# Kernel optimization log

Hardware: AMD Instinct MI355X
Metric: run time of the kernel (lower is better)

The kernel has to match this reference:

```python
import jax, jax.numpy as jnp
import numpy as np
import math

B, N, D, H = 16, 200, 2048, 2048  # batch, seq (== max_len), feature dim, hidden/output dim


def setup_inputs() -> dict:
    key = jax.random.key(0)
    ks = jax.random.split(key, 16)
    s = 1.0 / math.sqrt(D)
    return {
        "input_query": jax.random.normal(ks[0], (B, N, D), jnp.float32),
        "input_key": jax.random.normal(ks[1], (B, N, D), jnp.float32),
        "input_value": jax.random.normal(ks[2], (B, N, D), jnp.float32),
        "loc_vector": jax.random.normal(ks[3], (B, N, D), jnp.float32),
        "Wq": jax.random.normal(ks[4], (D, H), jnp.float32) * s,
        "bq": jnp.zeros((H,), jnp.float32),
        "Wk": jax.random.normal(ks[5], (D, H), jnp.float32) * s,
        "bk": jnp.zeros((H,), jnp.float32),
        "Wv": jax.random.normal(ks[6], (D, H), jnp.float32) * s,
        "bv": jnp.zeros((H,), jnp.float32),
        "Wloc": jax.random.normal(ks[7], (D, H), jnp.float32) * s,
        "bloc": jnp.zeros((H,), jnp.float32),
        "Wlk": jax.random.normal(ks[8], (D, H), jnp.float32) * s,
        "blk": jnp.zeros((H,), jnp.float32),
        "param": jax.random.normal(ks[9], (B, N, H), jnp.float32),
    }


def reference(input_query, input_key, input_value, loc_vector,
              Wq, bq, Wk, bk, Wv, bv, Wloc, bloc, Wlk, blk, param):
    n = input_query.shape[1]
    lq = input_query @ Wq + bq                      # (b, n, h)
    lk = input_key @ Wk + bk                        # (b, m, h)
    lv = input_value @ Wv + bv                      # (b, m, o)
    loc = loc_vector[:, :n, :]
    lloc = loc @ Wloc + bloc                        # (b, n, h)
    kloc = loc @ Wlk + blk                          # (b, n, h)
    p = param[: input_query.shape[0], :n, :]        # (b, n, h)
    # Fused multi-term scores: (Q+P)K^T + (Q+Lloc)Kloc^T  == QK^T + Lloc Kloc^T + P K^T + Q Kloc^T
    scores = (jnp.einsum('bnh,bmh->bnm', lq + p, lk)
              + jnp.einsum('bnh,bmh->bnm', lq + lloc, kloc))
    attn = jax.nn.softmax(scores / math.sqrt(lq.shape[-1]), axis=-1)
    return jnp.einsum('bnm,bmo->bno', attn, lv)     # (b, n, o); dropout is identity in eval
```

## Files before the change

kernel.cpp:

```cpp
#include <hip/hip_runtime.h>
#include <hip/hip_bf16.h>
#include <math.h>

typedef float floatx4 __attribute__((ext_vector_type(4)));
typedef __bf16 bf16x8 __attribute__((ext_vector_type(8)));
typedef unsigned short ushort_t;

__device__ __forceinline__ ushort_t f2bf(float f) {
    union { float f; unsigned int i; } v; v.f = f;
    unsigned int i = v.i;
    return (ushort_t)((i + 0x7FFFu + ((i >> 16) & 1u)) >> 16);
}
__device__ __forceinline__ unsigned int pack2(float a, float b) {
    return (unsigned int)f2bf(a) | ((unsigned int)f2bf(b) << 16);
}
__device__ __forceinline__ floatx4 mfma16(bf16x8 a, bf16x8 b, floatx4 c) {
    return __builtin_amdgcn_mfma_f32_16x16x32_bf16(a, b, c, 0, 0, 0);
}
__device__ __forceinline__ void load_lds16(const ushort_t* g, ushort_t* l) {
    __builtin_amdgcn_global_load_lds(
        (const __attribute__((address_space(1))) unsigned int*)g,
        (__attribute__((address_space(3))) unsigned int*)l, 16, 0, 0);
}

__global__ __launch_bounds__(256) void k_convert(const float* __restrict__ q, const float* __restrict__ k,
                          const float* __restrict__ v, const float* __restrict__ loc,
                          ushort_t* qb, ushort_t* kb, ushort_t* vb, ushort_t* locb) {
    int z = blockIdx.y;
    const float* src = z == 0 ? q : z == 1 ? k : z == 2 ? v : loc;
    ushort_t* dst    = z == 0 ? qb : z == 1 ? kb : z == 2 ? vb : locb;
    size_t idx = (size_t)blockIdx.x * 256 + threadIdx.x;
    floatx4 f = *(const floatx4*)(src + idx * 4);
    uint2 o;
    o.x = pack2(f[0], f[1]);
    o.y = pack2(f[2], f[3]);
    *(uint2*)(dst + idx * 4) = o;
}

__global__ void k_wtrans(const float* __restrict__ w0, const float* __restrict__ w1,
                         const float* __restrict__ w2, const float* __restrict__ w3,
                         const float* __restrict__ w4,
                         ushort_t* t0, ushort_t* t1, ushort_t* t2, ushort_t* t3, ushort_t* t4) {
    __shared__ float tile[32][33];
    int z = blockIdx.z;
    const float* W = z == 0 ? w0 : z == 1 ? w1 : z == 2 ? w2 : z == 3 ? w3 : w4;
    ushort_t* T    = z == 0 ? t0 : z == 1 ? t1 : z == 2 ? t2 : z == 3 ? t3 : t4;
    int n0 = blockIdx.x * 32, k0 = blockIdx.y * 32;
    int tx = threadIdx.x & 31, ty = threadIdx.x >> 5;
#pragma unroll
    for (int i = 0; i < 4; i++) {
        int row = ty + i * 8;
        tile[row][tx] = W[(size_t)(k0 + row) * 2048 + n0 + tx];
    }
    __syncthreads();
#pragma unroll
    for (int i = 0; i < 4; i++) {
        int row = ty + i * 8;
        T[(size_t)(n0 + row) * 2048 + k0 + tx] = f2bf(tile[tx][row]);
    }
}

__global__ void k_vtrans(const ushort_t* __restrict__ lv, ushort_t* __restrict__ lvT) {
    __shared__ ushort_t tile[32][33];
    int n0 = blockIdx.x * 32;
    int t0 = blockIdx.y * 32;
    int b = blockIdx.z;
    int tx = threadIdx.x & 31, ty = threadIdx.x >> 5;
#pragma unroll
    for (int i = 0; i < 4; i++) {
        int row = ty + i * 8;
        int tk = t0 + row;
        ushort_t v = 0;
        if (tk < 200) v = lv[(size_t)(b * 200 + tk) * 2048 + n0 + tx];
        tile[row][tx] = v;
    }
    __syncthreads();
#pragma unroll
    for (int i = 0; i < 4; i++) {
        int row = ty + i * 8;
        lvT[((size_t)b * 2048 + n0 + row) * 224 + t0 + tx] = tile[tx][row];
    }
}

#define G_SB  __builtin_amdgcn_sched_barrier(0)
#define G_BAR __builtin_amdgcn_s_barrier()

__global__ __launch_bounds__(512, 2) void k_gemm(
    const ushort_t* A0, const ushort_t* A1, const ushort_t* A2, const ushort_t* A3, const ushort_t* A4,
    const ushort_t* W0, const ushort_t* W1, const ushort_t* W2, const ushort_t* W3, const ushort_t* W4,
    const float* B0, const float* B1, const float* B2, const float* B3, const float* B4,
    ushort_t* lqp, ushort_t* lvp, ushort_t* llocp, ushort_t* kcat) {
    int wg = blockIdx.x;
    int swz = (wg & 7) * 65 + (wg >> 3);
    int z = swz / 104;
    int rem = swz - z * 104;
    int ntile = rem / 13;
    int mtile = rem - ntile * 13;
    int m0 = mtile * 256, n0 = ntile * 256;

    const ushort_t* A  = z == 0 ? A0 : z == 1 ? A1 : z == 2 ? A2 : z == 3 ? A3 : A4;
    const ushort_t* Wt = z == 0 ? W0 : z == 1 ? W1 : z == 2 ? W2 : z == 3 ? W3 : W4;
    const float* bias  = z == 0 ? B0 : z == 1 ? B1 : z == 2 ? B2 : z == 3 ? B3 : B4;

    __shared__ ushort_t As[2][256 * 32];
    __shared__ ushort_t Bs[2][256 * 32];

    int tid = threadIdx.x;
    int lane = tid & 63, w = tid >> 6;
    int quad = lane >> 4, col = lane & 15;
    int wr = w >> 2, wc = w & 3;

    int srow = lane >> 2;
    int cch  = (lane & 3) ^ ((lane >> 3) & 3);
    const ushort_t* AgB0 = A  + (size_t)(m0 + (0 * 8 + w) * 16 + srow) * 2048 + cch * 8;
    const ushort_t* AgB1 = A  + (size_t)(m0 + (1 * 8 + w) * 16 + srow) * 2048 + cch * 8;
    const ushort_t* BgB0 = Wt + (size_t)(n0 + (0 * 8 + w) * 16 + srow) * 2048 + cch * 8;
    const ushort_t* BgB1 = Wt + (size_t)(n0 + (1 * 8 + w) * 16 + srow) * 2048 + cch * 8;
    int dst0 = (0 * 8 + w) * 512;
    int dst1 = (1 * 8 + w) * 512;

#define G_STAGE(K0, B) do {                         \
        load_lds16(AgB0 + (K0), As[B] + dst0);      \
        load_lds16(AgB1 + (K0), As[B] + dst1);      \
        load_lds16(BgB0 + (K0), Bs[B] + dst0);      \
        load_lds16(BgB1 + (K0), Bs[B] + dst1);      \
    } while (0)

    int aoff[8], boff[4];
#pragma unroll
    for (int mi = 0; mi < 8; mi++) {
        int row = wr * 128 + mi * 16 + col;
        aoff[mi] = row * 32 + (quad ^ ((row >> 1) & 3)) * 8;
    }
#pragma unroll
    for (int ni = 0; ni < 4; ni++) {
        int row = wc * 64 + ni * 16 + col;
        boff[ni] = row * 32 + (quad ^ ((row >> 1) & 3)) * 8;
    }

    floatx4 acc[8][4] = {};

#define G_COMPUTE(B) do {                                                \
        bf16x8 af[8], bfr[4];                                            \
        _Pragma("unroll") for (int mi = 0; mi < 8; mi++)                 \
            af[mi] = *(const bf16x8*)&As[B][aoff[mi]];                   \
        _Pragma("unroll") for (int ni = 0; ni < 4; ni++)                 \
            bfr[ni] = *(const bf16x8*)&Bs[B][boff[ni]];                  \
        __builtin_amdgcn_s_setprio(1);                                   \
        _Pragma("unroll") for (int mi = 0; mi < 8; mi++)                 \
            _Pragma("unroll") for (int ni = 0; ni < 4; ni++)             \
                acc[mi][ni] = mfma16(af[mi], bfr[ni], acc[mi][ni]);      \
        __builtin_amdgcn_s_setprio(0);                                   \
    } while (0)

    G_STAGE(0, 0);

#pragma unroll 1
    for (int tt = 0; tt < 31; tt++) {
        int k0 = tt * 64;
        G_STAGE(k0 + 32, 1);
        asm volatile("s_waitcnt vmcnt(4)" ::: "memory");
        G_SB; G_BAR; G_SB;
        G_COMPUTE(0);
        G_SB; G_BAR;
        G_STAGE(k0 + 64, 0);
        asm volatile("s_waitcnt vmcnt(4)" ::: "memory");
        G_SB; G_BAR; G_SB;
        G_COMPUTE(1);
        G_SB; G_BAR;
    }
    G_STAGE(2016, 1);
    asm volatile("s_waitcnt vmcnt(4)" ::: "memory");
    G_SB; G_BAR; G_SB;
    G_COMPUTE(0);
    G_SB; G_BAR;
    asm volatile("s_waitcnt vmcnt(0)" ::: "memory");
    G_SB; G_BAR; G_SB;
    G_COMPUTE(1);

    ushort_t* Cplain = z == 0 ? lqp : z == 2 ? lvp : llocp;
    int kcoff = (z == 4) ? 2048 : 0;
    bool to_kcat = (z == 1 || z == 4);
    float bvv[4];
#pragma unroll
    for (int ni = 0; ni < 4; ni++) bvv[ni] = bias[n0 + wc * 64 + ni * 16 + col];
#pragma unroll
    for (int mi = 0; mi < 8; mi++) {
#pragma unroll
        for (int r = 0; r < 4; r++) {
            int m = m0 + wr * 128 + mi * 16 + quad * 4 + r;
            if (m < 3200) {
                ushort_t* crow;
                if (to_kcat) {
                    int bb = m / 200, rr = m - bb * 200;
                    crow = kcat + (size_t)(bb * 224 + rr) * 4096 + kcoff;
                } else {
                    crow = Cplain + (size_t)m * 2048;
                }
#pragma unroll
                for (int ni = 0; ni < 4; ni++) {
                    int n = n0 + wc * 64 + ni * 16 + col;
                    crow[n] = f2bf(acc[mi][ni][r] + bvv[ni]);
                }
            }
        }
    }
#undef G_STAGE
#undef G_COMPUTE
}

__global__ __launch_bounds__(256) void k_qprep(const ushort_t* __restrict__ lqp,
                                               const ushort_t* __restrict__ llocp,
                                               const float* __restrict__ param,
                                               ushort_t* __restrict__ qcat) {
    int m = blockIdx.x;
    int b = m / 200, r = m - b * 200;
    int c = threadIdx.x * 8;
    bf16x8 ql = *(const bf16x8*)(lqp + (size_t)m * 2048 + c);
    bf16x8 ll = *(const bf16x8*)(llocp + (size_t)m * 2048 + c);
    floatx4 p0 = *(const floatx4*)(param + (size_t)m * 2048 + c);
    floatx4 p1 = *(const floatx4*)(param + (size_t)m * 2048 + c + 4);
    bf16x8 q1, q2;
#pragma unroll
    for (int j = 0; j < 4; j++) {
        q1[j]     = (__bf16)((float)ql[j] + p0[j]);
        q1[j + 4] = (__bf16)((float)ql[j + 4] + p1[j]);
        q2[j]     = (__bf16)((float)ql[j] + (float)ll[j]);
        q2[j + 4] = (__bf16)((float)ql[j + 4] + (float)ll[j + 4]);
    }
    ushort_t* dst = qcat + ((size_t)(b * 224 + r)) * 4096 + c;
    *(bf16x8*)dst = q1;
    *(bf16x8*)(dst + 2048) = q2;
}

__global__ __launch_bounds__(256) void k_scores(const ushort_t* __restrict__ qcat,
                                                const ushort_t* __restrict__ kcat,
                                                float* __restrict__ part) {
    int qt = blockIdx.x;
    int b  = blockIdx.y;
    int kc = blockIdx.z;
    __shared__ ushort_t As[32 * 32];
    __shared__ ushort_t Bs[224 * 32];

    int tid = threadIdx.x;
    int lane = tid & 63, w = tid >> 6;
    int quad = lane >> 4, col = lane & 15;
    int srow = lane >> 2, scol = (lane & 3) * 8;

    const ushort_t* qbase = qcat + ((size_t)b * 224 + qt * 32) * 4096 + kc * 2048;
    const ushort_t* kbase = kcat + (size_t)b * 224 * 4096 + kc * 2048;

    const ushort_t* ssrc[4];
    ushort_t* sdst[4];
#pragma unroll
    for (int o = 0; o < 4; o++) {
        int id = w * 4 + o;
        if (id < 14) {
            ssrc[o] = kbase + (size_t)(id * 16 + srow) * 4096 + scol;
            sdst[o] = Bs + id * 512;
        } else {
            ssrc[o] = qbase + (size_t)((id - 14) * 16 + srow) * 4096 + scol;
            sdst[o] = As + (id - 14) * 512;
        }
    }

    floatx4 acc[2][4] = {};
    for (int k0 = 0; k0 < 2048; k0 += 32) {
        __syncthreads();
#pragma unroll
        for (int o = 0; o < 4; o++) load_lds16(ssrc[o] + k0, sdst[o]);
        __syncthreads();
        bf16x8 af[2];
#pragma unroll
        for (int mi = 0; mi < 2; mi++) af[mi] = *(const bf16x8*)&As[(mi * 16 + col) * 32 + quad * 8];
#pragma unroll
        for (int fi = 0; fi < 4; fi++) {
            int f = w + fi * 4;
            if (f < 14) {
                bf16x8 bf = *(const bf16x8*)&Bs[(f * 16 + col) * 32 + quad * 8];
#pragma unroll
                for (int mi = 0; mi < 2; mi++) acc[mi][fi] = mfma16(af[mi], bf, acc[mi][fi]);
            }
        }
    }

    float* pbase = part + ((size_t)(kc * 16 + b) * 224 + qt * 32) * 224;
#pragma unroll
    for (int fi = 0; fi < 4; fi++) {
        int f = w + fi * 4;
        if (f < 14) {
#pragma unroll
            for (int mi = 0; mi < 2; mi++)
#pragma unroll
                for (int r = 0; r < 4; r++)
                    pbase[(mi * 16 + quad * 4 + r) * 224 + f * 16 + col] = acc[mi][fi][r];
        }
    }
}

__global__ __launch_bounds__(256) void k_softmax(const float* __restrict__ part,
                                                 ushort_t* __restrict__ attn) {
    int row = blockIdx.x * 8 + (threadIdx.x >> 5);
    int b = row / 200, r = row - b * 200;
    int p = threadIdx.x & 31;
    const float* p0 = part + ((size_t)b * 224 + r) * 224;
    const float* p1 = p0 + (size_t)16 * 224 * 224;
    const float scale = 0.022097086912079608f;
    float ev[7];
    float mx = -1e30f;
#pragma unroll
    for (int j = 0; j < 7; j++) {
        int c = p * 7 + j;
        float v = (c < 200) ? (p0[c] + p1[c]) * scale : -1e30f;
        ev[j] = v;
        mx = fmaxf(mx, v);
    }
#pragma unroll
    for (int m = 1; m < 32; m <<= 1) mx = fmaxf(mx, __shfl_xor(mx, m, 32));
    float s = 0.f;
#pragma unroll
    for (int j = 0; j < 7; j++) {
        float e = __expf(ev[j] - mx);
        ev[j] = e;
        s += e;
    }
#pragma unroll
    for (int m = 1; m < 32; m <<= 1) s += __shfl_xor(s, m, 32);
    float rs = 1.0f / s;
    ushort_t* arow = attn + (size_t)row * 224;
#pragma unroll
    for (int j = 0; j < 7; j++) {
        int c = p * 7 + j;
        arow[c] = (c < 200) ? f2bf(ev[j] * rs) : (ushort_t)0;
    }
}

__global__ __launch_bounds__(256) void k_pv(const ushort_t* __restrict__ attn,
                                            const ushort_t* __restrict__ lvT,
                                            float* __restrict__ out) {
    int nt = blockIdx.x;
    int qt = blockIdx.y;
    int b = blockIdx.z;
    int tid = threadIdx.x, lane = tid & 63, w = tid >> 6;
    int quad = lane >> 4, col = lane & 15;
    int aq = qt * 16 + col; if (aq > 199) aq = 199;
    const ushort_t* arow = attn + (size_t)(b * 200 + aq) * 224;
    int nbase = nt * 128 + w * 32;
    const ushort_t* bp0 = lvT + ((size_t)b * 2048 + nbase + col) * 224;
    const ushort_t* bp1 = lvT + ((size_t)b * 2048 + nbase + 16 + col) * 224;
    floatx4 acc[2] = {};
#pragma unroll
    for (int k0 = 0; k0 < 224; k0 += 32) {
        int ko = k0 + quad * 8;
        bf16x8 av = *(const bf16x8*)(arow + ko);
        bf16x8 b0 = *(const bf16x8*)(bp0 + ko);
        bf16x8 b1 = *(const bf16x8*)(bp1 + ko);
        acc[0] = mfma16(av, b0, acc[0]);
        acc[1] = mfma16(av, b1, acc[1]);
    }
#pragma unroll
    for (int f = 0; f < 2; f++) {
        int n = nbase + f * 16 + col;
#pragma unroll
        for (int r = 0; r < 4; r++) {
            int m = qt * 16 + quad * 4 + r;
            if (m < 200) out[(size_t)(b * 200 + m) * 2048 + n] = acc[f][r];
        }
    }
}

extern "C" void kernel_launch(void* const* d_in, const int* in_sizes, int n_in,
                              void* d_out, int out_size, void* d_ws, size_t ws_size,
                              hipStream_t stream) {
    (void)in_sizes; (void)n_in; (void)out_size; (void)ws_size;
    const float* q    = (const float*)d_in[0];
    const float* k    = (const float*)d_in[1];
    const float* v    = (const float*)d_in[2];
    const float* loc  = (const float*)d_in[3];
    const float* Wq   = (const float*)d_in[4];
    const float* bq   = (const float*)d_in[5];
    const float* Wk   = (const float*)d_in[6];
    const float* bk   = (const float*)d_in[7];
    const float* Wv   = (const float*)d_in[8];
    const float* bv   = (const float*)d_in[9];
    const float* Wloc = (const float*)d_in[10];
    const float* bloc = (const float*)d_in[11];
    const float* Wlk  = (const float*)d_in[12];
    const float* blk  = (const float*)d_in[13];
    const float* param = (const float*)d_in[14];
    float* out = (float*)d_out;

    size_t off = 0;
    auto nxt = [&](size_t bytes) {
        void* p = (char*)d_ws + off;
        off += (bytes + 255) & ~(size_t)255;
        return p;
    };
    ushort_t* wt[5];
    for (int i = 0; i < 5; i++) wt[i] = (ushort_t*)nxt(2048ull * 2048 * 2);
    ushort_t* qb    = (ushort_t*)nxt(3200ull * 2048 * 2);
    ushort_t* kb    = (ushort_t*)nxt(3200ull * 2048 * 2);
    ushort_t* vb    = (ushort_t*)nxt(3200ull * 2048 * 2);
    ushort_t* locb  = (ushort_t*)nxt(3200ull * 2048 * 2);
    ushort_t* lqp   = (ushort_t*)nxt(3200ull * 2048 * 2);
    ushort_t* llocp = (ushort_t*)nxt(3200ull * 2048 * 2);
    ushort_t* lvp   = (ushort_t*)nxt(3200ull * 2048 * 2);
    ushort_t* kcat  = (ushort_t*)nxt(16ull * 224 * 4096 * 2);
    ushort_t* lvT  = wt[0];
    ushort_t* attn = wt[0] + 16ull * 2048 * 224;
    float*    part = (float*)((char*)d_ws + 2ull * 2048 * 2048 * 2);
    ushort_t* qcat = qb;

    k_convert<<<dim3(6400, 4), 256, 0, stream>>>(q, k, v, loc, qb, kb, vb, locb);
    k_wtrans<<<dim3(64, 64, 5), 256, 0, stream>>>(Wq, Wk, Wv, Wloc, Wlk,
                                                  wt[0], wt[1], wt[2], wt[3], wt[4]);
    k_gemm<<<dim3(520), 512, 0, stream>>>(qb, kb, vb, locb, locb,
                                          wt[0], wt[1], wt[2], wt[3], wt[4],
                                          bq, bk, bv, bloc, blk,
                                          lqp, lvp, llocp, kcat);
    k_qprep<<<dim3(3200), 256, 0, stream>>>(lqp, llocp, param, qcat);
    k_vtrans<<<dim3(64, 7, 16), 256, 0, stream>>>(lvp, lvT);
    k_scores<<<dim3(7, 16, 2), 256, 0, stream>>>(qcat, kcat, part);
    k_softmax<<<dim3(400), 256, 0, stream>>>(part, attn);
    k_pv<<<dim3(16, 13, 16), 256, 0, stream>>>(attn, lvT, out);
}
```

Measured before the change: 515.8 us.

## Restructure projection GEMM main loop into 64-wide K tiles with quadrant-split pipeline

The projection GEMM now stages 64-wide K tiles instead of 32-wide ones, using an XOR swizzle across 8 chunks. Each K step is split into four quadrant MFMA phases, with LDS fragment reads and partial global-to-LDS loads for the next tiles interleaved between barriers. The aim is to overlap LDS reads and global loads with MFMA work and to halve the number of loop iterations. In exchange there are more barriers per iteration, LDS use doubles (which may limit the 2 blocks/CU occupancy), and the asynchronous buffer reuse carries correctness risk. The wraparound tile indices issue a few redundant loads at the tail.

Result: slower. 535.5 us (+3.8%).

```diff
diff --git a/kernel.cpp b/kernel.cpp
--- a/kernel.cpp
+++ b/kernel.cpp
@@ -82,8 +82,12 @@
     }
 }
 
-#define G_SB  __builtin_amdgcn_sched_barrier(0)
-#define G_BAR __builtin_amdgcn_s_barrier()
+#define G_SB   __builtin_amdgcn_sched_barrier(0)
+#define G_BAR  __builtin_amdgcn_s_barrier()
+#define WAITL0 asm volatile("s_waitcnt lgkmcnt(0)" ::: "memory")
+#define WAITL8 asm volatile("s_waitcnt lgkmcnt(8)" ::: "memory")
+#define WVM4   asm volatile("s_waitcnt vmcnt(4)" ::: "memory")
+#define WVM0   asm volatile("s_waitcnt vmcnt(0)" ::: "memory")
 
 __global__ __launch_bounds__(512, 2) void k_gemm(
     const ushort_t* A0, const ushort_t* A1, const ushort_t* A2, const ushort_t* A3, const ushort_t* A4,
@@ -102,81 +106,99 @@
     const ushort_t* Wt = z == 0 ? W0 : z == 1 ? W1 : z == 2 ? W2 : z == 3 ? W3 : W4;
     const float* bias  = z == 0 ? B0 : z == 1 ? B1 : z == 2 ? B2 : z == 3 ? B3 : B4;
 
-    __shared__ ushort_t As[2][256 * 32];
-    __shared__ ushort_t Bs[2][256 * 32];
+    __shared__ ushort_t AsF[2 * 256 * 64];
+    __shared__ ushort_t BsF[2 * 256 * 64];
 
     int tid = threadIdx.x;
     int lane = tid & 63, w = tid >> 6;
     int quad = lane >> 4, col = lane & 15;
     int wr = w >> 2, wc = w & 3;
 
-    int srow = lane >> 2;
-    int cch  = (lane & 3) ^ ((lane >> 3) & 3);
-    const ushort_t* AgB0 = A  + (size_t)(m0 + (0 * 8 + w) * 16 + srow) * 2048 + cch * 8;
-    const ushort_t* AgB1 = A  + (size_t)(m0 + (1 * 8 + w) * 16 + srow) * 2048 + cch * 8;
-    const ushort_t* BgB0 = Wt + (size_t)(n0 + (0 * 8 + w) * 16 + srow) * 2048 + cch * 8;
-    const ushort_t* BgB1 = Wt + (size_t)(n0 + (1 * 8 + w) * 16 + srow) * 2048 + cch * 8;
-    int dst0 = (0 * 8 + w) * 512;
-    int dst1 = (1 * 8 + w) * 512;
-
-#define G_STAGE(K0, B) do {                         \
-        load_lds16(AgB0 + (K0), As[B] + dst0);      \
-        load_lds16(AgB1 + (K0), As[B] + dst1);      \
-        load_lds16(BgB0 + (K0), Bs[B] + dst0);      \
-        load_lds16(BgB1 + (K0), Bs[B] + dst1);      \
-    } while (0)
-
-    int aoff[8], boff[4];
-#pragma unroll
-    for (int mi = 0; mi < 8; mi++) {
-        int row = wr * 128 + mi * 16 + col;
-        aoff[mi] = row * 32 + (quad ^ ((row >> 1) & 3)) * 8;
-    }
-#pragma unroll
-    for (int ni = 0; ni < 4; ni++) {
-        int row = wc * 64 + ni * 16 + col;
-        boff[ni] = row * 32 + (quad ^ ((row >> 1) & 3)) * 8;
-    }
-
+    int sl = lane >> 3;
+    int sc = ((lane & 7) ^ sl) * 8;
+    const ushort_t* Ag[4]; const ushort_t* Bg[4]; int ldst[4];
+#pragma unroll
+    for (int u = 0; u < 4; u++) {
+        int rowoff = (u >> 1) * 128 + (u & 1) * 64 + w * 8;
+        Ag[u] = A  + (size_t)(m0 + rowoff + sl) * 2048 + sc;
+        Bg[u] = Wt + (size_t)(n0 + rowoff + sl) * 2048 + sc;
+        ldst[u] = rowoff * 64;
+    }
+
+#define STG_A(KT, BUF) do { int kk = (KT) * 64;                       \
+        load_lds16(Ag[0] + kk, AsF + (BUF) * 16384 + ldst[0]);        \
+        load_lds16(Ag[1] + kk, AsF + (BUF) * 16384 + ldst[1]);        \
+        load_lds16(Ag[2] + kk, AsF + (BUF) * 16384 + ldst[2]);        \
+        load_lds16(Ag[3] + kk, AsF + (BUF) * 16384 + ldst[3]); } while (0)
+#define STG_BLO(KT, BUF) do { int kk = (KT) * 64;                     \
+        load_lds16(Bg[0] + kk, BsF + (BUF) * 16384 + ldst[0]);        \
+        load_lds16(Bg[1] + kk, BsF + (BUF) * 16384 + ldst[1]); } while (0)
+#define STG_BHI(KT, BUF) do { int kk = (KT) * 64;                     \
+        load_lds16(Bg[2] + kk, BsF + (BUF) * 16384 + ldst[2]);        \
+        load_lds16(Bg[3] + kk, BsF + (BUF) * 16384 + ldst[3]); } while (0)
+
+    int sw = col & 7;
+    int ko0 = (quad ^ sw) * 8;
+    int ko1 = ((4 | quad) ^ sw) * 8;
+    int aro[8], bro[4];
+#pragma unroll
+    for (int mi = 0; mi < 8; mi++) aro[mi] = (wr * 128 + mi * 16 + col) * 64;
+#pragma unroll
+    for (int ni = 0; ni < 4; ni++) bro[ni] = (wc * 64 + ni * 16 + col) * 64;
+
+    bf16x8 af[4][2], bfr[2][2];
     floatx4 acc[8][4] = {};
 
-#define G_COMPUTE(B) do {                                                \
-        bf16x8 af[8], bfr[4];                                            \
-        _Pragma("unroll") for (int mi = 0; mi < 8; mi++)                 \
-            af[mi] = *(const bf16x8*)&As[B][aoff[mi]];                   \
-        _Pragma("unroll") for (int ni = 0; ni < 4; ni++)                 \
-            bfr[ni] = *(const bf16x8*)&Bs[B][boff[ni]];                  \
-        __builtin_amdgcn_s_setprio(1);                                   \
-        _Pragma("unroll") for (int mi = 0; mi < 8; mi++)                 \
-            _Pragma("unroll") for (int ni = 0; ni < 4; ni++)             \
-                acc[mi][ni] = mfma16(af[mi], bfr[ni], acc[mi][ni]);      \
-        __builtin_amdgcn_s_setprio(0);                                   \
-    } while (0)
-
-    G_STAGE(0, 0);
+#define RD_A(J, MI, BUF) do {                                         \
+        const ushort_t* p_ = AsF + (BUF) * 16384 + aro[MI];           \
+        af[J][0] = *(const bf16x8*)(p_ + ko0);                        \
+        af[J][1] = *(const bf16x8*)(p_ + ko1); } while (0)
+#define RD_B(J, NI, BUF) do {                                         \
+        const ushort_t* p_ = BsF + (BUF) * 16384 + bro[NI];           \
+        bfr[J][0] = *(const bf16x8*)(p_ + ko0);                       \
+        bfr[J][1] = *(const bf16x8*)(p_ + ko1); } while (0)
+#define QMFMA(MH, NB) do {                                            \
+        __builtin_amdgcn_s_setprio(1);                                \
+        _Pragma("unroll") for (int mi = 0; mi < 4; mi++)              \
+        _Pragma("unroll") for (int nj = 0; nj < 2; nj++) {            \
+            acc[(MH) * 4 + mi][(NB) + nj] =                           \
+                mfma16(af[mi][0], bfr[nj][0], acc[(MH) * 4 + mi][(NB) + nj]); \
+            acc[(MH) * 4 + mi][(NB) + nj] =                           \
+                mfma16(af[mi][1], bfr[nj][1], acc[(MH) * 4 + mi][(NB) + nj]); } \
+        __builtin_amdgcn_s_setprio(0); } while (0)
+
+    STG_A(0, 0); STG_BLO(0, 0); STG_BHI(0, 0); STG_A(1, 1);
+    WVM4; G_SB; G_BAR; G_SB;
 
 #pragma unroll 1
-    for (int tt = 0; tt < 31; tt++) {
-        int k0 = tt * 64;
-        G_STAGE(k0 + 32, 1);
-        asm volatile("s_waitcnt vmcnt(4)" ::: "memory");
-        G_SB; G_BAR; G_SB;
-        G_COMPUTE(0);
+    for (int t = 0; t < 32; t++) {
+        int c = t & 1, o = c ^ 1;
+        int tB = (t + 1) & 31;
+        int tA = (t + 2) & 31;
+        RD_A(0, 0, c); RD_A(1, 1, c); RD_A(2, 2, c); RD_A(3, 3, c);
+        RD_B(0, 0, c); RD_B(1, 1, c);
+        STG_BLO(tB, o);
+        WAITL8;
+        G_SB; G_BAR; WAITL0; G_SB;
+        QMFMA(0, 0);
         G_SB; G_BAR;
-        G_STAGE(k0 + 64, 0);
-        asm volatile("s_waitcnt vmcnt(4)" ::: "memory");
-        G_SB; G_BAR; G_SB;
-        G_COMPUTE(1);
+        RD_B(0, 2, c); RD_B(1, 3, c);
+        STG_BHI(tB, o);
+        G_SB; G_BAR; WAITL0; G_SB;
+        QMFMA(0, 2);
         G_SB; G_BAR;
-    }
-    G_STAGE(2016, 1);
-    asm volatile("s_waitcnt vmcnt(4)" ::: "memory");
-    G_SB; G_BAR; G_SB;
-    G_COMPUTE(0);
-    G_SB; G_BAR;
-    asm volatile("s_waitcnt vmcnt(0)" ::: "memory");
-    G_SB; G_BAR; G_SB;
-    G_COMPUTE(1);
+        RD_A(0, 4, c); RD_A(1, 5, c); RD_A(2, 6, c); RD_A(3, 7, c);
+        G_SB; G_BAR; WAITL0; G_SB;
+        QMFMA(1, 2);
+        G_SB; G_BAR;
+        RD_B(0, 0, c); RD_B(1, 1, c);
+        STG_A(tA, c);
+        WVM4;
+        G_SB; G_BAR; WAITL0; G_SB;
+        QMFMA(1, 0);
+        G_SB; G_BAR;
+    }
+    WVM0;
 
     ushort_t* Cplain = z == 0 ? lqp : z == 2 ? lvp : llocp;
     int kcoff = (z == 4) ? 2048 : 0;
@@ -205,8 +227,12 @@
             }
         }
     }
-#undef G_STAGE
-#undef G_COMPUTE
+#undef STG_A
+#undef STG_BLO
+#undef STG_BHI
+#undef RD_A
+#undef RD_B
+#undef QMFMA
 }
 
 __global__ __launch_bounds__(256) void k_qprep(const ushort_t* __restrict__ lqp,
```
